# Kernel tuning notes

Measured on AMD Instinct MI355X. Metric: run time of the kernel, lower is better.

Reference implementation:

```python
import jax, jax.numpy as jnp
import numpy as np

C = 512
GROUPS = 32
EPS = 1e-6


def setup_inputs() -> dict:
    key = jax.random.key(0)
    ks = jax.random.split(key, 10)
    B, H, W = 4, 64, 64
    s = 1.0 / np.sqrt(C)
    return {
        "x": jax.random.normal(ks[0], (B, C, H, W), dtype=jnp.float32),
        "gn_weight": jnp.ones((C,), jnp.float32),
        "gn_bias": jnp.zeros((C,), jnp.float32),
        "Wq": jax.random.normal(ks[1], (C, C), jnp.float32) * s,
        "bq": jnp.zeros((C,), jnp.float32),
        "Wk": jax.random.normal(ks[2], (C, C), jnp.float32) * s,
        "bk": jnp.zeros((C,), jnp.float32),
        "Wv": jax.random.normal(ks[3], (C, C), jnp.float32) * s,
        "bv": jnp.zeros((C,), jnp.float32),
        "Wo": jax.random.normal(ks[4], (C, C), jnp.float32) * s,
        "bo": jnp.zeros((C,), jnp.float32),
    }


def _group_norm(x, weight, bias):
    B, Ch, H, W = x.shape
    xg = x.reshape(B, GROUPS, Ch // GROUPS, H, W)
    mean = jnp.mean(xg, axis=(2, 3, 4), keepdims=True)
    var = jnp.var(xg, axis=(2, 3, 4), keepdims=True)
    xg = (xg - mean) * jax.lax.rsqrt(var + EPS)
    h = xg.reshape(B, Ch, H, W)
    return h * weight[None, :, None, None] + bias[None, :, None, None]


def reference(x, gn_weight, gn_bias, Wq, bq, Wk, bk, Wv, bv, Wo, bo):
    B, Ch, H, W = x.shape
    h = _group_norm(x, gn_weight, gn_bias)
    # [B, N, C] with N = H*W spatial tokens
    h = h.reshape(B, Ch, H * W).transpose(0, 2, 1)
    q = h @ Wq.T + bq
    k = h @ Wk.T + bk
    v = h @ Wv.T + bv
    scale = 1.0 / jnp.sqrt(jnp.asarray(Ch, x.dtype))
    scores = jnp.einsum("bnc,bmc->bnm", q, k) * scale  # [B, N, N]
    attn = jax.nn.softmax(scores, axis=-1)
    out = jnp.einsum("bnm,bmc->bnc", attn, v)
    out = out @ Wo.T + bo  # Dropout(0.0) is identity
    out = out.transpose(0, 2, 1).reshape(B, Ch, H, W)
    return x + out
```

## Files before the change

### kernel.cpp

```cpp
#include <hip/hip_runtime.h>
#include <hip/hip_bf16.h>

typedef __attribute__((ext_vector_type(8))) short bf16x8;
typedef __attribute__((ext_vector_type(4))) short bf16x4;
typedef __attribute__((ext_vector_type(4))) float f32x4;

__device__ __forceinline__ short f2bf(float f){
  __hip_bfloat16 h = __float2bfloat16(f);
  return __builtin_bit_cast(short, h);
}
__device__ __forceinline__ float bf2f(short s){
  unsigned u = ((unsigned)(unsigned short)s) << 16;
  return __builtin_bit_cast(float, u);
}

__device__ __forceinline__ void gload_lds16(const short* g, char* l){
  __builtin_amdgcn_global_load_lds(
      (const __attribute__((address_space(1))) void*)g,
      (__attribute__((address_space(3))) void*)l, 16, 0, 0);
}

#define SB0() __builtin_amdgcn_sched_barrier(0)

__global__ __launch_bounds__(256) void gn_stats(const float* __restrict__ x,
                                                float* __restrict__ stats){
  int b = blockIdx.x >> 5, g = blockIdx.x & 31;
  const float4* p = (const float4*)(x + ((long long)b*512 + g*16)*4096);
  float s = 0.f, s2 = 0.f;
  for (int i = threadIdx.x; i < 16384; i += 256){
    float4 v = p[i];
    s  += v.x + v.y + v.z + v.w;
    s2 += v.x*v.x + v.y*v.y + v.z*v.z + v.w*v.w;
  }
  #pragma unroll
  for (int o = 32; o; o >>= 1){ s += __shfl_xor(s, o); s2 += __shfl_xor(s2, o); }
  __shared__ float rs[4], rs2[4];
  int wid = threadIdx.x >> 6;
  if ((threadIdx.x & 63) == 0){ rs[wid] = s; rs2[wid] = s2; }
  __syncthreads();
  if (threadIdx.x == 0){
    float S  = rs[0]+rs[1]+rs[2]+rs[3];
    float S2 = rs2[0]+rs2[1]+rs2[2]+rs2[3];
    float mean = S * (1.f/65536.f);
    float var  = S2 * (1.f/65536.f) - mean*mean;
    stats[blockIdx.x*2]   = mean;
    stats[blockIdx.x*2+1] = rsqrtf(var + 1e-6f);
  }
}

__global__ __launch_bounds__(256) void gn_apply(const float* __restrict__ x,
                                                const float* __restrict__ stats,
                                                const float* __restrict__ gw,
                                                const float* __restrict__ gb,
                                                short* __restrict__ h){
  __shared__ float tile[128][65];
  int b  = blockIdx.y;
  int n0 = blockIdx.x * 64;
  int t  = threadIdx.x;
  const float* xb = x + (long long)b*512*4096;
  for (int cc = 0; cc < 4; cc++){
    int c0 = cc*128;
    #pragma unroll
    for (int r = 0; r < 128; r += 4){
      int c = r + (t >> 6);
      tile[c][t & 63] = xb[(long long)(c0+c)*4096 + n0 + (t & 63)];
    }
    __syncthreads();
    int n = t >> 2, cp = (t & 3)*32;
    short tmp[32];
    #pragma unroll
    for (int j = 0; j < 32; j++){
      int c = c0 + cp + j;
      float mean = stats[(b*32 + (c >> 4))*2];
      float rstd = stats[(b*32 + (c >> 4))*2 + 1];
      float v = (tile[cp+j][n] - mean)*rstd*gw[c] + gb[c];
      tmp[j] = f2bf(v);
    }
    long long ho = ((long long)b*4096 + n0 + n)*512 + c0 + cp;
    #pragma unroll
    for (int j2 = 0; j2 < 4; j2++){
      bf16x8 v8;
      #pragma unroll
      for (int e = 0; e < 8; e++) v8[e] = tmp[j2*8 + e];
      *(bf16x8*)&h[ho + j2*8] = v8;
    }
    __syncthreads();
  }
}

__global__ __launch_bounds__(256) void f2bf_all(
    const float* __restrict__ w0, const float* __restrict__ w1,
    const float* __restrict__ w2, const float* __restrict__ w3,
    short* __restrict__ o0, short* __restrict__ o1,
    short* __restrict__ o2, short* __restrict__ o3){
  int idx = blockIdx.x*256 + threadIdx.x;
  int m = idx >> 15, r = idx & 32767;
  const float* src = (m==0) ? w0 : (m==1) ? w1 : (m==2) ? w2 : w3;
  short* dst       = (m==0) ? o0 : (m==1) ? o1 : (m==2) ? o2 : o3;
  const float4* p = (const float4*)src + (long long)r*2;
  float4 a = p[0], c = p[1];
  bf16x8 v;
  v[0]=f2bf(a.x); v[1]=f2bf(a.y); v[2]=f2bf(a.z); v[3]=f2bf(a.w);
  v[4]=f2bf(c.x); v[5]=f2bf(c.y); v[6]=f2bf(c.z); v[7]=f2bf(c.w);
  *(bf16x8*)&dst[(long long)r*8] = v;
}

__global__ __launch_bounds__(256) void bcat(const float* __restrict__ bq,
                                            const float* __restrict__ bk,
                                            const float* __restrict__ bv,
                                            float* __restrict__ o){
  int t = blockIdx.x*256 + threadIdx.x;
  if (t < 512){ o[t] = bq[t]; o[512+t] = bk[t]; o[1024+t] = bv[t]; }
}

__global__ __launch_bounds__(256) void reduce_den(const float* __restrict__ partial,
                                                  float* __restrict__ inv_den,
                                                  int nrows){
  int r = blockIdx.x*256 + threadIdx.x;
  if (r >= nrows) return;
  const float4* p = (const float4*)(partial + (long long)r*16);
  float4 a = p[0], b = p[1], c = p[2], d = p[3];
  float s = a.x+a.y+a.z+a.w + b.x+b.y+b.z+b.w + c.x+c.y+c.z+c.w + d.x+d.y+d.z+d.w;
  inv_den[r] = 1.f / s;
}

template<int MODE, int TM, int BN, int TH, int SWZ>
__global__ __launch_bounds__(TH, 2) void gemmF(
    const short* __restrict__ A, const short* __restrict__ Bw,
    const float* __restrict__ bias,
    void* __restrict__ outp, const float* __restrict__ resid,
    int M, int Nn, int Kd,
    long long sA, long long sB, long long sO, float scale,
    const float* __restrict__ dptr, float* __restrict__ partial)
{
  constexpr int WAVES   = TH/64;
  constexpr int WARPS_N = BN/64;
  constexpr int WARPS_M = WAVES/WARPS_N;
  constexpr int WM = TM/WARPS_M;
  constexpr int MF = WM/16;
  constexpr int ABYT = TM*128;
  constexpr int BUFSZ = (TM+BN)*128;
  constexpr int APASS = (TM*128)/(TH*16);
  constexpr int BPASS = (BN*128)/(TH*16);
  constexpr int LOADS = APASS + BPASS;
  extern __shared__ char smem[];

  int bx, by, bz;
  if constexpr (SWZ == 1){
    int id = blockIdx.x;
    int xcd = id & 7, s = id >> 3;
    int region = xcd + ((s >> 4) << 3);
    int o = s & 15;
    bz = region >> 4;
    bx = (region & 3)*4 + (o & 3);
    by = ((region >> 2) & 3)*4 + (o >> 2);
  } else if constexpr (SWZ == 2){
    int id = blockIdx.x;
    int xcd = id & 7, s = id >> 3;
    int combo = xcd*2 + (s & 1);
    by = combo & 3; bz = combo >> 2;
    bx = s >> 1;
  } else { bx = blockIdx.x; by = blockIdx.y; bz = blockIdx.z; }

  const short* Ab = A + bz*sA;
  const short* Bb = Bw + bz*sB;
  const int m0 = bx*TM, n0 = by*BN;
  const int t = threadIdx.x;
  const int lane = t & 63, wid = t >> 6;
  const int g = lane >> 4, lr = lane & 15;
  const int wr = wid / WARPS_N, wc = wid % WARPS_N;
  const long long KdLL = Kd;

  auto STAGE = [&](int kt, int buf){
    char* d0 = smem + buf*BUFSZ;
    #pragma unroll
    for (int p = 0; p < APASS; p++){
      int f = p*TH*16 + t*16;
      int row = f >> 7, ch = (f >> 4) & 7;
      gload_lds16(Ab + (long long)(m0+row)*KdLL + (long long)kt*64 + ((ch ^ (row&7))*8),
                  d0 + f);
    }
    #pragma unroll
    for (int p = 0; p < BPASS; p++){
      int f = p*TH*16 + t*16;
      int row = f >> 7, ch = (f >> 4) & 7;
      gload_lds16(Bb + (long long)(n0+row)*KdLL + (long long)kt*64 + ((ch ^ (row&7))*8),
                  d0 + ABYT + f);
    }
  };

  int roA[MF], swA[MF], roB[4], swB[4];
  #pragma unroll
  for (int mf = 0; mf < MF; mf++){
    int ra = wr*WM + mf*16 + lr;
    roA[mf] = ra*128; swA[mf] = ra & 7;
  }
  #pragma unroll
  for (int nf = 0; nf < 4; nf++){
    int rb = wc*64 + nf*16 + lr;
    roB[nf] = ABYT + rb*128; swB[nf] = rb & 7;
  }

  f32x4 acc[MF][4];
  #pragma unroll
  for (int i = 0; i < MF; i++)
    #pragma unroll
    for (int j = 0; j < 4; j++)
      acc[i][j] = f32x4{0.f,0.f,0.f,0.f};

  const int NT = Kd >> 6;

  STAGE(0, 0);
  STAGE(1, 1);
  if constexpr (LOADS == 8) asm volatile("s_waitcnt vmcnt(8)":::"memory");
  else                      asm volatile("s_waitcnt vmcnt(6)":::"memory");
  SB0();
  __builtin_amdgcn_s_barrier();

  for (int kt = 0; kt < NT; ++kt){
    char* base = smem + (kt & 1)*BUFSZ;
    bf16x8 av[MF][2], bv[4][2];
    #pragma unroll
    for (int n = 0; n < 4; n++)
      #pragma unroll
      for (int ks = 0; ks < 2; ks++)
        bv[n][ks] = *(const bf16x8*)(base + roB[n] + (((ks*4+g) ^ swB[n])<<4));
    #pragma unroll
    for (int m = 0; m < MF; m++)
      #pragma unroll
      for (int ks = 0; ks < 2; ks++)
        av[m][ks] = *(const bf16x8*)(base + roA[m] + (((ks*4+g) ^ swA[m])<<4));
    #pragma unroll
    for (int ks = 0; ks < 2; ks++)
      #pragma unroll
      for (int m = 0; m < MF; m++)
        #pragma unroll
        for (int n = 0; n < 4; n++){
          if constexpr (MODE == 2)
            acc[m][n] = __builtin_amdgcn_mfma_f32_16x16x32_bf16(av[m][ks], bv[n][ks], acc[m][n], 0,0,0);
          else
            acc[m][n] = __builtin_amdgcn_mfma_f32_16x16x32_bf16(bv[n][ks], av[m][ks], acc[m][n], 0,0,0);
        }
    SB0();
    __builtin_amdgcn_s_barrier();
    SB0();
    if (kt + 2 < NT){
      STAGE(kt + 2, kt & 1);
      if constexpr (LOADS == 8) asm volatile("s_waitcnt vmcnt(8)":::"memory");
      else                      asm volatile("s_waitcnt vmcnt(6)":::"memory");
    } else {
      asm volatile("s_waitcnt vmcnt(0)":::"memory");
    }
    __builtin_amdgcn_s_barrier();
  }

  if constexpr (MODE == 4){
    short* outb = (short*)outp + bz*sO;
    float* rowpart = (float*)smem;
    constexpr float LOG2E = 1.4426950408889634f;
    #pragma unroll
    for (int mi = 0; mi < MF; mi++){
      int lrow = wr*WM + mi*16 + lr;
      int row  = m0 + lrow;
      float rs = 0.f;
      #pragma unroll
      for (int ni = 0; ni < 4; ni++){
        int col = n0 + wc*64 + ni*16 + g*4;
        bf16x4 pk;
        #pragma unroll
        for (int i = 0; i < 4; i++){
          float p = exp2f(acc[mi][ni][i]*LOG2E);
          rs += p;
          pk[i] = f2bf(p);
        }
        *(bf16x4*)&outb[(long long)row*Nn + col] = pk;
      }
      rs += __shfl_xor(rs, 16);
      rs += __shfl_xor(rs, 32);
      if (g == 0) rowpart[lrow*WARPS_N + wc] = rs;
    }
    __syncthreads();
    if (t < TM){
      float s2 = 0.f;
      #pragma unroll
      for (int j = 0; j < WARPS_N; j++) s2 += rowpart[t*WARPS_N + j];
      partial[((long long)bz*4096 + m0 + t)*16 + by] = s2;
    }
  } else if constexpr (MODE == 5){
    short* outb = (short*)outp + bz*sO;
    const float* dd = dptr + (long long)bz*M;
    #pragma unroll
    for (int mi = 0; mi < MF; mi++){
      int row = m0 + wr*WM + mi*16 + lr;
      float inv = dd[row];
      #pragma unroll
      for (int ni = 0; ni < 4; ni++){
        int col = n0 + wc*64 + ni*16 + g*4;
        bf16x4 pk;
        #pragma unroll
        for (int i = 0; i < 4; i++) pk[i] = f2bf(acc[mi][ni][i]*inv);
        *(bf16x4*)&outb[(long long)row*Nn + col] = pk;
      }
    }
  } else if constexpr (MODE == 6){
    const int seg = by >> 2;
    const long long base = (long long)bz*sO;
    short* qp  = (short*)outp;
    short* kp  = (short*)partial;
    short* vtp = (short*)dptr;
    #pragma unroll
    for (int mi = 0; mi < MF; mi++){
      int row = m0 + wr*WM + mi*16 + lr;
      #pragma unroll
      for (int ni = 0; ni < 4; ni++){
        int col = n0 + wc*64 + ni*16 + g*4;
        float4 bb = *(const float4*)&bias[col];
        int cq = col - seg*512;
        float sc = (seg == 0) ? scale : 1.f;
        bf16x4 pk;
        pk[0] = f2bf((acc[mi][ni][0] + bb.x)*sc);
        pk[1] = f2bf((acc[mi][ni][1] + bb.y)*sc);
        pk[2] = f2bf((acc[mi][ni][2] + bb.z)*sc);
        pk[3] = f2bf((acc[mi][ni][3] + bb.w)*sc);
        if (seg == 0)      *(bf16x4*)&qp[base + (long long)row*512 + cq] = pk;
        else if (seg == 1) *(bf16x4*)&kp[base + (long long)row*512 + cq] = pk;
        else {
          #pragma unroll
          for (int i = 0; i < 4; i++)
            vtp[base + (long long)(cq+i)*4096 + row] = pk[i];
        }
      }
    }
  } else {
    float* outb = (float*)outp + bz*sO;
    const float* rx = resid + bz*sO;
    #pragma unroll
    for (int ni = 0; ni < 4; ni++){
      int col = n0 + wc*64 + ni*16 + lr;
      float bv2 = bias[col];
      #pragma unroll
      for (int mi = 0; mi < MF; mi++){
        int row = m0 + wr*WM + mi*16 + g*4;
        long long off = (long long)col*M + row;
        float4 xr = *(const float4*)&rx[off];
        float4 o;
        o.x = acc[mi][ni][0] + bv2 + xr.x;
        o.y = acc[mi][ni][1] + bv2 + xr.y;
        o.z = acc[mi][ni][2] + bv2 + xr.z;
        o.w = acc[mi][ni][3] + bv2 + xr.w;
        *(float4*)&outb[off] = o;
      }
    }
  }
}

extern "C" void kernel_launch(void* const* d_in, const int* in_sizes, int n_in,
                              void* d_out, int out_size, void* d_ws, size_t ws_size,
                              hipStream_t stream)
{
  const float* x   = (const float*)d_in[0];
  const float* gnw = (const float*)d_in[1];
  const float* gnb = (const float*)d_in[2];
  const float* Wq  = (const float*)d_in[3];
  const float* bq  = (const float*)d_in[4];
  const float* Wk  = (const float*)d_in[5];
  const float* bk  = (const float*)d_in[6];
  const float* Wv  = (const float*)d_in[7];
  const float* bvp = (const float*)d_in[8];
  const float* Wo  = (const float*)d_in[9];
  const float* bo  = (const float*)d_in[10];
  float* out = (float*)d_out;

  char* ws = (char*)d_ws;
  const size_t MB = 1ull << 20;
  short* h      = (short*)(ws);
  short* q      = (short*)(ws + 16*MB);
  short* kmat   = (short*)(ws + 32*MB);
  short* vt     = (short*)(ws + 48*MB);
  short* ao     = (short*)(ws + 64*MB);
  short* wqkv   = (short*)(ws + 80*MB);
  short* wob    = wqkv + 3*262144;
  float* stats  = (float*)(ws + 82*MB);
  float* inv_den= (float*)(ws + 82*MB + 8192);
  float* bqkv   = (float*)(ws + 82*MB + 131072);
  float* partial= (float*)(ws + 83*MB);
  short* S      = (short*)(ws + 84*MB);

  const int LDS_SC = 131072;
  const int LDS_QK = 98304;
  const int LDS_PV = 65536;
  hipFuncSetAttribute(reinterpret_cast<const void*>(&gemmF<4,256,256,512,1>),
                      hipFuncAttributeMaxDynamicSharedMemorySize, LDS_SC);
  hipFuncSetAttribute(reinterpret_cast<const void*>(&gemmF<4,256,256,512,0>),
                      hipFuncAttributeMaxDynamicSharedMemorySize, LDS_SC);
  hipFuncSetAttribute(reinterpret_cast<const void*>(&gemmF<6,256,128,512,0>),
                      hipFuncAttributeMaxDynamicSharedMemorySize, LDS_QK);
  hipFuncSetAttribute(reinterpret_cast<const void*>(&gemmF<5,128,128,256,2>),
                      hipFuncAttributeMaxDynamicSharedMemorySize, LDS_PV);
  hipFuncSetAttribute(reinterpret_cast<const void*>(&gemmF<5,128,128,256,0>),
                      hipFuncAttributeMaxDynamicSharedMemorySize, LDS_PV);
  hipFuncSetAttribute(reinterpret_cast<const void*>(&gemmF<2,128,128,256,0>),
                      hipFuncAttributeMaxDynamicSharedMemorySize, LDS_PV);

  dim3 blk(256);
  dim3 blk512(512);
  gn_stats<<<dim3(128), blk, 0, stream>>>(x, stats);
  gn_apply<<<dim3(64,4), blk, 0, stream>>>(x, stats, gnw, gnb, h);
  f2bf_all<<<dim3(512), blk, 0, stream>>>(Wq, Wk, Wv, Wo, wqkv, wqkv + 262144, wqkv + 2*262144, wob);
  bcat<<<dim3(2), blk, 0, stream>>>(bq, bk, bvp, bqkv);

  const long long sTok = 4096ll*512;
  const long long sS   = 4096ll*4096;
  const float qscale = 0.044194173824159216f;

  gemmF<6,256,128,512,0><<<dim3(16,12,4), blk512, LDS_QK, stream>>>(
      h, wqkv, bqkv, q, nullptr, 4096, 1536, 512, sTok, 0, sTok, qscale,
      (const float*)vt, (float*)kmat);

  if (ws_size >= 212*MB){
    gemmF<4,256,256,512,1><<<dim3(1024), blk512, LDS_SC, stream>>>(
        q, kmat, nullptr, S, nullptr, 4096, 4096, 512, sTok, sTok, sS, 1.f, nullptr, partial);
    reduce_den<<<dim3(64), blk, 0, stream>>>(partial, inv_den, 16384);
    gemmF<5,128,128,256,2><<<dim3(512), blk, LDS_PV, stream>>>(
        S, vt, nullptr, ao, nullptr, 4096, 512, 4096, sS, sTok, sTok, 1.f, inv_den, nullptr);
  } else {
    for (int b = 0; b < 4; b++){
      gemmF<4,256,256,512,0><<<dim3(16,16,1), blk512, LDS_SC, stream>>>(
          q + b*sTok, kmat + b*sTok, nullptr, S, nullptr, 4096, 4096, 512, 0, 0, 0, 1.f, nullptr, partial);
      reduce_den<<<dim3(16), blk, 0, stream>>>(partial, inv_den, 4096);
      gemmF<5,128,128,256,0><<<dim3(32,4,1), blk, LDS_PV, stream>>>(
          S, vt + b*sTok, nullptr, ao + b*sTok, nullptr, 4096, 512, 4096, 0, 0, 0, 1.f, inv_den, nullptr);
    }
  }

  gemmF<2,128,128,256,0><<<dim3(32,4,4), blk, LDS_PV, stream>>>(
      ao, wob, bo, out, x, 4096, 512, 512, sTok, 0, sTok, 1.f, nullptr, nullptr);
}
```

Baseline: 298.7 us.

## Add dedicated 8-phase pipelined QK^T score kernel with exp epilogue

Replaces the generic templated score GEMM (mode 4, 256x256 tiles) with a specialized kernel that splits each K-tile into four half-tile stages for A and B. These stages are interleaved with quarter-tile MFMA phases under setprio, explicit lgkmcnt/vmcnt waits and barriers. The goal is to overlap global-to-LDS loads with matrix math and hide LDS read latency better than the previous double-buffered loop. The epilogue exponentiates the scores, writes bf16 probabilities and records per-row partial sums. It adds many barriers per K-step, and correctness depends on the hand-tuned wait counts.

```diff
diff --git a/kernel.cpp b/kernel.cpp
--- a/kernel.cpp
+++ b/kernel.cpp
@@ -122,6 +122,280 @@
   float4 a = p[0], b = p[1], c = p[2], d = p[3];
   float s = a.x+a.y+a.z+a.w + b.x+b.y+b.z+b.w + c.x+c.y+c.z+c.w + d.x+d.y+d.z+d.w;
   inv_den[r] = 1.f / s;
+}
+
+__global__ __launch_bounds__(512, 2) void gemm8(
+    const short* __restrict__ A, const short* __restrict__ Bw,
+    short* __restrict__ outp,
+    int Nn, int Kd,
+    long long sA, long long sB, long long sO,
+    float* __restrict__ partial)
+{
+  constexpr int BUFSZ = 65536;
+  extern __shared__ char smem[];
+
+  int id = blockIdx.x;
+  int xcd = id & 7, s = id >> 3;
+  int region = xcd + ((s >> 4) << 3);
+  int o = s & 15;
+  const int bz = region >> 4;
+  const int bx = (region & 3)*4 + (o & 3);
+  const int by = ((region >> 2) & 3)*4 + (o >> 2);
+
+  const short* Ab = A + bz*sA;
+  const short* Bb = Bw + bz*sB;
+  const int m0 = bx*256, n0 = by*256;
+  const int t = threadIdx.x;
+  const int lane = t & 63, wid = t >> 6;
+  const int g = lane >> 4, lr = lane & 15;
+  const int wr = wid >> 2, wc = wid & 3;
+  const long long KdLL = Kd;
+
+  auto STG = [&](int kt, int buf, int which){
+    const bool isB = which >= 2;
+    const int h = which & 1;
+    char* d = smem + buf*BUFSZ + (isB ? 32768 : 0) + h*16384 + t*16;
+    const short* src = isB ? Bb : Ab;
+    const int base = isB ? n0 : m0;
+    #pragma unroll
+    for (int p = 0; p < 2; p++){
+      int row = h*128 + p*64 + (t >> 3);
+      int ch = t & 7;
+      gload_lds16(src + (long long)(base+row)*KdLL + (long long)kt*64 + ((ch ^ (row&7))*8),
+                  d + p*8192);
+    }
+  };
+
+  int roA[8], swA[8], roB[4], swB[4];
+  #pragma unroll
+  for (int mf = 0; mf < 8; mf++){
+    int ra = wr*128 + mf*16 + lr;
+    roA[mf] = ra*128; swA[mf] = ra & 7;
+  }
+  #pragma unroll
+  for (int nf = 0; nf < 4; nf++){
+    int rb = wc*64 + nf*16 + lr;
+    roB[nf] = 32768 + rb*128; swB[nf] = rb & 7;
+  }
+
+  f32x4 acc[8][4];
+  #pragma unroll
+  for (int i = 0; i < 8; i++)
+    #pragma unroll
+    for (int j = 0; j < 4; j++)
+      acc[i][j] = f32x4{0.f,0.f,0.f,0.f};
+
+  bf16x8 av[4][2], bv[4][2];
+
+  #define RD_A(QM, BASE)                                                   \
+    _Pragma("unroll")                                                      \
+    for (int _i = 0; _i < 4; _i++)                                         \
+      _Pragma("unroll")                                                    \
+      for (int _ks = 0; _ks < 2; _ks++)                                    \
+        av[_i][_ks] = *(const bf16x8*)((BASE) + roA[(QM)*4+_i] +           \
+                       (((_ks*4+g) ^ swA[(QM)*4+_i])<<4));
+  #define RD_B(QN, BASE)                                                   \
+    _Pragma("unroll")                                                      \
+    for (int _j = 0; _j < 2; _j++)                                         \
+      _Pragma("unroll")                                                    \
+      for (int _ks = 0; _ks < 2; _ks++)                                    \
+        bv[(QN)*2+_j][_ks] = *(const bf16x8*)((BASE) + roB[(QN)*2+_j] +    \
+                       (((_ks*4+g) ^ swB[(QN)*2+_j])<<4));
+  #define MFMA16(QN)                                                       \
+    __builtin_amdgcn_s_setprio(1);                                         \
+    _Pragma("unroll")                                                      \
+    for (int _ks = 0; _ks < 2; _ks++)                                      \
+      _Pragma("unroll")                                                    \
+      for (int _m = 0; _m < 4; _m++)                                       \
+        _Pragma("unroll")                                                  \
+        for (int _j = 0; _j < 2; _j++)                                     \
+          accp[_m][(QN)*2+_j] = __builtin_amdgcn_mfma_f32_16x16x32_bf16(   \
+            bv[(QN)*2+_j][_ks], av[_m][_ks], accp[_m][(QN)*2+_j], 0,0,0);  \
+    __builtin_amdgcn_s_setprio(0);
+
+  #define LGKM0() asm volatile("s_waitcnt lgkmcnt(0)" ::: "memory")
+  #define LGKM8() asm volatile("s_waitcnt lgkmcnt(8)" ::: "memory")
+  #define VM4()   asm volatile("s_waitcnt vmcnt(4)" ::: "memory")
+  #define VM0()   asm volatile("s_waitcnt vmcnt(0)" ::: "memory")
+  #define BAR()   __builtin_amdgcn_s_barrier()
+
+  const int NT = Kd >> 6;
+  const int NI = NT >> 1;
+
+  STG(0,0,0); STG(0,0,1); STG(0,0,2); STG(0,0,3);
+  STG(1,1,2); STG(1,1,3);
+  VM4();
+  BAR();
+
+  for (int i = 0; i < NI; ++i){
+    const int kt0 = 2*i, kt1 = kt0 + 1;
+    char* bc = smem + (kt0 & 1)*BUFSZ;
+    char* bn = smem + (kt1 & 1)*BUFSZ;
+    {
+      f32x4 (&accp)[8][4] = acc;
+      RD_A(0, bc); RD_B(0, bc);
+      if (kt1 < NT) STG(kt1, kt1 & 1, 0);
+      LGKM8();
+      BAR();
+      LGKM0();
+      { f32x4 (&accp2)[8][4] = acc; (void)accp2; }
+      __builtin_amdgcn_s_setprio(1);
+      #pragma unroll
+      for (int _ks = 0; _ks < 2; _ks++)
+        #pragma unroll
+        for (int _m = 0; _m < 4; _m++)
+          #pragma unroll
+          for (int _j = 0; _j < 2; _j++)
+            acc[_m][_j] = __builtin_amdgcn_mfma_f32_16x16x32_bf16(
+              bv[_j][_ks], av[_m][_ks], acc[_m][_j], 0,0,0);
+      __builtin_amdgcn_s_setprio(0);
+      BAR();
+      RD_B(1, bc);
+      if (kt1 < NT) STG(kt1, kt1 & 1, 1);
+      BAR();
+      LGKM0();
+      __builtin_amdgcn_s_setprio(1);
+      #pragma unroll
+      for (int _ks = 0; _ks < 2; _ks++)
+        #pragma unroll
+        for (int _m = 0; _m < 4; _m++)
+          #pragma unroll
+          for (int _j = 2; _j < 4; _j++)
+            acc[_m][_j] = __builtin_amdgcn_mfma_f32_16x16x32_bf16(
+              bv[_j][_ks], av[_m][_ks], acc[_m][_j], 0,0,0);
+      __builtin_amdgcn_s_setprio(0);
+      BAR();
+      RD_A(1, bc);
+      if (kt0+2 < NT) STG(kt0+2, kt0 & 1, 2);
+      BAR();
+      LGKM0();
+      __builtin_amdgcn_s_setprio(1);
+      #pragma unroll
+      for (int _ks = 0; _ks < 2; _ks++)
+        #pragma unroll
+        for (int _m = 0; _m < 4; _m++)
+          #pragma unroll
+          for (int _j = 0; _j < 2; _j++)
+            acc[4+_m][_j] = __builtin_amdgcn_mfma_f32_16x16x32_bf16(
+              bv[_j][_ks], av[_m][_ks], acc[4+_m][_j], 0,0,0);
+      __builtin_amdgcn_s_setprio(0);
+      BAR();
+      if (kt0+2 < NT) STG(kt0+2, kt0 & 1, 3);
+      BAR();
+      __builtin_amdgcn_s_setprio(1);
+      #pragma unroll
+      for (int _ks = 0; _ks < 2; _ks++)
+        #pragma unroll
+        for (int _m = 0; _m < 4; _m++)
+          #pragma unroll
+          for (int _j = 2; _j < 4; _j++)
+            acc[4+_m][_j] = __builtin_amdgcn_mfma_f32_16x16x32_bf16(
+              bv[_j][_ks], av[_m][_ks], acc[4+_m][_j], 0,0,0);
+      __builtin_amdgcn_s_setprio(0);
+      if (kt1 < NT) VM4(); else VM0();
+      BAR();
+    }
+    if (kt1 < NT){
+      RD_A(0, bn); RD_B(0, bn);
+      if (kt0+2 < NT) STG(kt0+2, kt0 & 1, 0);
+      LGKM8();
+      BAR();
+      LGKM0();
+      __builtin_amdgcn_s_setprio(1);
+      #pragma unroll
+      for (int _ks = 0; _ks < 2; _ks++)
+        #pragma unroll
+        for (int _m = 0; _m < 4; _m++)
+          #pragma unroll
+          for (int _j = 0; _j < 2; _j++)
+            acc[_m][_j] = __builtin_amdgcn_mfma_f32_16x16x32_bf16(
+              bv[_j][_ks], av[_m][_ks], acc[_m][_j], 0,0,0);
+      __builtin_amdgcn_s_setprio(0);
+      BAR();
+      RD_B(1, bn);
+      if (kt0+2 < NT) STG(kt0+2, kt0 & 1, 1);
+      BAR();
+      LGKM0();
+      __builtin_amdgcn_s_setprio(1);
+      #pragma unroll
+      for (int _ks = 0; _ks < 2; _ks++)
+        #pragma unroll
+        for (int _m = 0; _m < 4; _m++)
+          #pragma unroll
+          for (int _j = 2; _j < 4; _j++)
+            acc[_m][_j] = __builtin_amdgcn_mfma_f32_16x16x32_bf16(
+              bv[_j][_ks], av[_m][_ks], acc[_m][_j], 0,0,0);
+      __builtin_amdgcn_s_setprio(0);
+      BAR();
+      RD_A(1, bn);
+      if (kt1+2 < NT) STG(kt1+2, kt1 & 1, 2);
+      BAR();
+      LGKM0();
+      __builtin_amdgcn_s_setprio(1);
+      #pragma unroll
+      for (int _ks = 0; _ks < 2; _ks++)
+        #pragma unroll
+        for (int _m = 0; _m < 4; _m++)
+          #pragma unroll
+          for (int _j = 0; _j < 2; _j++)
+            acc[4+_m][_j] = __builtin_amdgcn_mfma_f32_16x16x32_bf16(
+              bv[_j][_ks], av[_m][_ks], acc[4+_m][_j], 0,0,0);
+      __builtin_amdgcn_s_setprio(0);
+      BAR();
+      if (kt1+2 < NT) STG(kt1+2, kt1 & 1, 3);
+      BAR();
+      __builtin_amdgcn_s_setprio(1);
+      #pragma unroll
+      for (int _ks = 0; _ks < 2; _ks++)
+        #pragma unroll
+        for (int _m = 0; _m < 4; _m++)
+          #pragma unroll
+          for (int _j = 2; _j < 4; _j++)
+            acc[4+_m][_j] = __builtin_amdgcn_mfma_f32_16x16x32_bf16(
+              bv[_j][_ks], av[_m][_ks], acc[4+_m][_j], 0,0,0);
+      __builtin_amdgcn_s_setprio(0);
+      if (kt1+2 < NT) VM4(); else VM0();
+      BAR();
+    }
+  }
+
+  short* outb = outp + bz*sO;
+  float* rowpart = (float*)smem;
+  constexpr float LOG2E = 1.4426950408889634f;
+  #pragma unroll
+  for (int mi = 0; mi < 8; mi++){
+    int lrow = wr*128 + mi*16 + lr;
+    int row  = m0 + lrow;
+    float rs = 0.f;
+    #pragma unroll
+    for (int ni = 0; ni < 4; ni++){
+      int col = n0 + wc*64 + ni*16 + g*4;
+      bf16x4 pk;
+      #pragma unroll
+      for (int i2 = 0; i2 < 4; i2++){
+        float p = exp2f(acc[mi][ni][i2]*LOG2E);
+        rs += p;
+        pk[i2] = f2bf(p);
+      }
+      *(bf16x4*)&outb[(long long)row*Nn + col] = pk;
+    }
+    rs += __shfl_xor(rs, 16);
+    rs += __shfl_xor(rs, 32);
+    if (g == 0) rowpart[lrow*4 + wc] = rs;
+  }
+  __syncthreads();
+  if (t < 256){
+    float s2 = rowpart[t*4] + rowpart[t*4+1] + rowpart[t*4+2] + rowpart[t*4+3];
+    partial[((long long)bz*4096 + m0 + t)*16 + by] = s2;
+  }
+  #undef RD_A
+  #undef RD_B
+  #undef MFMA16
+  #undef LGKM0
+  #undef LGKM8
+  #undef VM4
+  #undef VM0
+  #undef BAR
 }
 
 template<int MODE, int TM, int BN, int TH, int SWZ>
@@ -146,15 +420,7 @@
   extern __shared__ char smem[];
 
   int bx, by, bz;
-  if constexpr (SWZ == 1){
-    int id = blockIdx.x;
-    int xcd = id & 7, s = id >> 3;
-    int region = xcd + ((s >> 4) << 3);
-    int o = s & 15;
-    bz = region >> 4;
-    bx = (region & 3)*4 + (o & 3);
-    by = ((region >> 2) & 3)*4 + (o >> 2);
-  } else if constexpr (SWZ == 2){
+  if constexpr (SWZ == 2){
     int id = blockIdx.x;
     int xcd = id & 7, s = id >> 3;
     int combo = xcd*2 + (s & 1);
@@ -386,11 +652,12 @@
   float* partial= (float*)(ws + 83*MB);
   short* S      = (short*)(ws + 84*MB);
 
+  const int LDS_8P = 131072;
   const int LDS_SC = 131072;
   const int LDS_QK = 98304;
   const int LDS_PV = 65536;
-  hipFuncSetAttribute(reinterpret_cast<const void*>(&gemmF<4,256,256,512,1>),
-                      hipFuncAttributeMaxDynamicSharedMemorySize, LDS_SC);
+  hipFuncSetAttribute(reinterpret_cast<const void*>(&gemm8),
+                      hipFuncAttributeMaxDynamicSharedMemorySize, LDS_8P);
   hipFuncSetAttribute(reinterpret_cast<const void*>(&gemmF<4,256,256,512,0>),
                       hipFuncAttributeMaxDynamicSharedMemorySize, LDS_SC);
   hipFuncSetAttribute(reinterpret_cast<const void*>(&gemmF<6,256,128,512,0>),
@@ -418,8 +685,8 @@
       (const float*)vt, (float*)kmat);
 
   if (ws_size >= 212*MB){
-    gemmF<4,256,256,512,1><<<dim3(1024), blk512, LDS_SC, stream>>>(
-        q, kmat, nullptr, S, nullptr, 4096, 4096, 512, sTok, sTok, sS, 1.f, nullptr, partial);
+    gemm8<<<dim3(1024), blk512, LDS_8P, stream>>>(
+        q, kmat, S, 4096, 512, sTok, sTok, sS, partial);
     reduce_den<<<dim3(64), blk, 0, stream>>>(partial, inv_den, 16384);
     gemmF<5,128,128,256,2><<<dim3(512), blk, LDS_PV, stream>>>(
         S, vt, nullptr, ao, nullptr, 4096, 512, 4096, sS, sTok, sTok, 1.f, inv_den, nullptr);
```

Result: no change. 295.5 us (-1.1%).
